# Performance work log

Measured on AMD Instinct MI355X. Metric: run time of the kernel, lower is better.

## Reference

```python
import jax, jax.numpy as jnp
import numpy as np

T, B = 64, 2048
LATENT, OBS, CTRL, NMAT, H = 128, 128, 16, 16, 128


def setup_inputs() -> dict:
    key = jax.random.key(0)
    ks = iter(jax.random.split(key, 32))

    def dense(shape, fan_in):
        return jax.random.normal(next(ks), shape, jnp.float32) / np.sqrt(fan_in)

    inp = {
        "xs": jax.random.normal(next(ks), (T, B, OBS), jnp.float32),
        "us": jax.random.normal(next(ks), (T, B, CTRL), jnp.float32),
        "eps1": jax.random.normal(next(ks), (B, LATENT), jnp.float32),
        "eps": jax.random.normal(next(ks), (T - 1, B, LATENT), jnp.float32),
        # InitialNetwork: LSTM(128) + Dense(128) + Dense(2*latent)
        "lstm_Wx": dense((OBS, 4 * H), OBS),
        "lstm_Wh": dense((H, 4 * H), H),
        "lstm_b": jnp.zeros((4 * H,), jnp.float32),
        "init_W1": dense((H, H), H),
        "init_b1": jnp.zeros((H,), jnp.float32),
        "init_W2": dense((H, 2 * LATENT), H),
        "init_b2": jnp.zeros((2 * LATENT,), jnp.float32),
        # InitialTransition
        "trans_W1": dense((LATENT, H), LATENT),
        "trans_b1": jnp.zeros((H,), jnp.float32),
        "trans_W2": dense((H, LATENT), H),
        "trans_b2": jnp.zeros((LATENT,), jnp.float32),
        # Observation
        "obs_W1": dense((LATENT, H), LATENT),
        "obs_b1": jnp.zeros((H,), jnp.float32),
        "obs_W2": dense((H, OBS), H),
        "obs_b2": jnp.zeros((OBS,), jnp.float32),
        # Recognition (input: z ++ x ++ u)
        "rec_W1": dense((LATENT + OBS + CTRL, H), LATENT + OBS + CTRL),
        "rec_b1": jnp.zeros((H,), jnp.float32),
        "rec_W2": dense((H, 2 * LATENT), H),
        "rec_b2": jnp.zeros((2 * LATENT,), jnp.float32),
        # TransitionWeights (no bias, normal(0.01) init)
        "alpha_W": 0.01 * jax.random.normal(next(ks), (LATENT + CTRL, NMAT), jnp.float32),
        # mixture banks
        "A": 0.01 * jax.random.normal(next(ks), (NMAT, LATENT, LATENT), jnp.float32),
        "Bm": 0.01 * jax.random.normal(next(ks), (NMAT, LATENT, CTRL), jnp.float32),
        "C": 0.01 * jax.random.normal(next(ks), (NMAT, OBS, LATENT), jnp.float32),
    }
    return inp


def reference(xs, us, eps1, eps, lstm_Wx, lstm_Wh, lstm_b,
              init_W1, init_b1, init_W2, init_b2,
              trans_W1, trans_b1, trans_W2, trans_b2,
              obs_W1, obs_b1, obs_W2, obs_b2,
              rec_W1, rec_b1, rec_W2, rec_b2,
              alpha_W, A, Bm, C):
    Bsz = xs.shape[1]
    Hd = lstm_Wh.shape[0]

    # --- InitialNetwork: LSTM over time (xs is (T,B,obs); flax transposes to batch-major, net effect is a scan over T) ---
    def lstm_step(carry, x_t):
        c, h = carry
        gates = x_t @ lstm_Wx + h @ lstm_Wh + lstm_b  # (B, 4H)
        i, f, g, o = jnp.split(gates, 4, axis=-1)     # flax gate order i,f,g,o
        c = jax.nn.sigmoid(f) * c + jax.nn.sigmoid(i) * jnp.tanh(g)
        h = jax.nn.sigmoid(o) * jnp.tanh(c)
        return (c, h), None

    zeros = jnp.zeros((Bsz, Hd), xs.dtype)
    (_, h_last), _ = jax.lax.scan(lstm_step, (zeros, zeros), xs)
    hid = jax.nn.relu(h_last @ init_W1 + init_b1)
    w1_mean, w1_logvar = jnp.split(hid @ init_W2 + init_b2, 2, axis=-1)
    w_1 = w1_mean + jnp.exp(w1_logvar / 2) * eps1

    # --- InitialTransition ---
    z_1 = jax.nn.relu(w_1 @ trans_W1 + trans_b1) @ trans_W2 + trans_b2

    def obs_fn(z):
        return jax.nn.relu(z @ obs_W1 + obs_b1) @ obs_W2 + obs_b2

    # --- unrolled DVBF transition as a scan over t = 0..T-2 ---
    def step(z, inp):
        x_next, u_t, eps_t = inp
        x_mean = obs_fn(z)
        r = jax.nn.relu(jnp.concatenate([z, x_next, u_t], axis=-1) @ rec_W1 + rec_b1)
        w_mean, w_logvar = jnp.split(r @ rec_W2 + rec_b2, 2, axis=-1)
        w = w_mean + jnp.exp(w_logvar / 2) * eps_t
        alphas = jax.nn.softmax(jnp.concatenate([z, u_t], axis=-1) @ alpha_W)  # (B, NMAT)
        # fused gating + matrix mixing + matvec (same math as building A_t/B_t/C_t)
        z_next = (jnp.einsum('bi,ijk,bk->bj', alphas, A, z)
                  + jnp.einsum('bi,ijk,bk->bj', alphas, Bm, u_t)
                  + jnp.einsum('bi,ijk,bk->bj', alphas, C, w))
        return z_next, (z_next, x_mean)

    Tn = xs.shape[0]
    _, (zs_rest, x_rec) = jax.lax.scan(step, z_1, (xs[1:], us[:Tn - 1], eps[:Tn - 1]))

    zs = jnp.concatenate([z_1[None], zs_rest], axis=0).reshape(-1, z_1.shape[-1])  # vstack -> (T*B, latent)
    x_rec = x_rec.reshape(-1, x_rec.shape[-1])                                    # ((T-1)*B, obs)
    return zs, x_rec
```

## Files before the change

### kernel.cpp

```cpp
#include <hip/hip_runtime.h>
#include <math.h>

#define TT   64
#define BB   2048
#define OBSN 128
#define CTRLN 16
#define LATN 128
#define NMN  16
#define HDN  128

typedef __attribute__((ext_vector_type(8))) short short8;
typedef __attribute__((ext_vector_type(4))) float f32x4;

__device__ __forceinline__ float sigf(float x) { return 1.0f / (1.0f + expf(-x)); }

__device__ __forceinline__ unsigned short f2bf(float x) {
    unsigned int u = __float_as_uint(x);
    unsigned int r = (u + 0x7fffu + ((u >> 16) & 1u)) >> 16;
    return (unsigned short)r;
}

__device__ __forceinline__ f32x4 mfma16(short8 a, short8 b, f32x4 c) {
    return __builtin_amdgcn_mfma_f32_16x16x32_bf16(a, b, c, 0, 0, 0);
}

__global__ __launch_bounds__(256) void cvt_bf4_k(
    const float* __restrict__ in, unsigned short* __restrict__ out, int n4)
{
    int i = blockIdx.x * 256 + threadIdx.x;
    if (i >= n4) return;
    float4 v = ((const float4*)in)[i];
    ushort4 o;
    o.x = f2bf(v.x); o.y = f2bf(v.y); o.z = f2bf(v.z); o.w = f2bf(v.w);
    ((ushort4*)out)[i] = o;
}

__global__ __launch_bounds__(256) void pack_b_k(
    const float* __restrict__ W, unsigned short* __restrict__ out,
    int K, int N, int KT)
{
    int id = blockIdx.x * 256 + threadIdx.x;
    int total = (N / 16) * KT * 64;
    if (id >= total) return;
    int lane = id & 63;
    int kt = (id >> 6) % KT;
    int nt = id / (64 * KT);
    int n = nt * 16 + (lane & 15);
    int kb = kt * 32 + (lane >> 4) * 8;
#pragma unroll
    for (int j = 0; j < 8; j++) {
        int k = kb + j;
        out[(size_t)id * 8 + j] = (k < K) ? f2bf(W[(size_t)k * N + n]) : (unsigned short)0;
    }
}

__global__ __launch_bounds__(256) void pack_lstm_k(
    const float* __restrict__ Wx, const float* __restrict__ Wh,
    unsigned short* __restrict__ out)
{
    int id = blockIdx.x * 256 + threadIdx.x;
    if (id >= 32 * 8 * 64) return;
    int lane = id & 63;
    int kt = (id >> 6) & 7;
    int nt = id >> 9;
    int n = nt * 16 + (lane & 15);
    int kb = kt * 32 + (lane >> 4) * 8;
#pragma unroll
    for (int j = 0; j < 8; j++) {
        int k = kb + j;
        float v = (k < 128) ? Wx[(size_t)k * 512 + n] : Wh[(size_t)(k - 128) * 512 + n];
        out[(size_t)id * 8 + j] = f2bf(v);
    }
}

__global__ __launch_bounds__(256) void pack_wmix_k(
    const float* __restrict__ A, const float* __restrict__ Bm,
    const float* __restrict__ C, unsigned short* __restrict__ out)
{
    int id = blockIdx.x * 256 + threadIdx.x;
    if (id >= 128 * 9 * 64) return;
    int lane = id & 63;
    int kt = (id >> 6) % 9;
    int nt = id / (64 * 9);
    int c = nt * 16 + (lane & 15);
    int i = c >> 7, jj = c & 127;
    int kb = kt * 32 + (lane >> 4) * 8;
#pragma unroll
    for (int j = 0; j < 8; j++) {
        int k = kb + j;
        float v;
        if (k < 128)      v = A[((size_t)(i * 128 + jj)) * 128 + k];
        else if (k < 144) v = Bm[(size_t)(i * 128 + jj) * 16 + (k - 128)];
        else if (k < 272) v = C[(size_t)(i * 128 + jj) * 128 + (k - 144)];
        else              v = 0.f;
        out[(size_t)id * 8 + j] = f2bf(v);
    }
}

__global__ __launch_bounds__(512) void lstm_k(
    const unsigned short* __restrict__ xs_bf,
    const unsigned short* __restrict__ lstm_pk,
    const float* __restrict__ bias,
    float* __restrict__ hlast)
{
    __shared__ unsigned short h_bf[16][136];
    __shared__ float cs[16][128];
    __shared__ float gb[16][516];
    __shared__ float bs[512];

    const int tid = threadIdx.x;
    const int lane = tid & 63;
    const int w = tid >> 6;
    const int quad = lane >> 4;
    const int l15 = lane & 15;
    const int row0 = blockIdx.x * 16;

    bs[tid] = bias[tid];
    for (int idx = tid; idx < 16 * 136; idx += 512) h_bf[idx / 136][idx % 136] = 0;
    for (int idx = tid; idx < 2048; idx += 512) cs[idx >> 7][idx & 127] = 0.f;
    __syncthreads();

    for (int t = 0; t < TT; t++) {
        short8 a[8];
#pragma unroll
        for (int kt = 0; kt < 4; kt++)
            a[kt] = *(const short8*)&xs_bf[((size_t)t * 2048 + row0 + l15) * 128 + kt * 32 + quad * 8];
#pragma unroll
        for (int kt = 4; kt < 8; kt++)
            a[kt] = *(const short8*)&h_bf[l15][(kt - 4) * 32 + quad * 8];

        f32x4 D[4];
#pragma unroll
        for (int s = 0; s < 4; s++) D[s] = (f32x4){0.f, 0.f, 0.f, 0.f};
#pragma unroll
        for (int kt = 0; kt < 8; kt++) {
#pragma unroll
            for (int s = 0; s < 4; s++) {
                int ntg = w * 4 + s;
                short8 b = *(const short8*)&lstm_pk[(((size_t)ntg * 8 + kt) * 64 + lane) * 8];
                D[s] = mfma16(a[kt], b, D[s]);
            }
        }
#pragma unroll
        for (int s = 0; s < 4; s++)
#pragma unroll
            for (int rg = 0; rg < 4; rg++)
                gb[quad * 4 + rg][(w * 4 + s) * 16 + l15] = D[s][rg];
        __syncthreads();

#pragma unroll
        for (int e = 0; e < 4; e++) {
            int idx = tid + e * 512;
            int r = idx >> 7, j = idx & 127;
            float gi = gb[r][j] + bs[j];
            float gf = gb[r][128 + j] + bs[128 + j];
            float gg = gb[r][256 + j] + bs[256 + j];
            float go = gb[r][384 + j] + bs[384 + j];
            float c = sigf(gf) * cs[r][j] + sigf(gi) * tanhf(gg);
            float h = sigf(go) * tanhf(c);
            cs[r][j] = c;
            h_bf[r][j] = f2bf(h);
            if (t == TT - 1) hlast[(size_t)(row0 + r) * 128 + j] = h;
        }
        __syncthreads();
    }
}

__global__ __launch_bounds__(512) void scan_k(
    const unsigned short* __restrict__ xs_bf,
    const unsigned short* __restrict__ us_bf,
    const float* __restrict__ eps,
    const unsigned short* __restrict__ rec1_pk,
    const float* __restrict__ rec_b1,
    const unsigned short* __restrict__ rec2_pk,
    const float* __restrict__ rec_b2,
    const unsigned short* __restrict__ alpha_pk,
    const unsigned short* __restrict__ wmix_pk,
    float* __restrict__ zs)
{
    __shared__ unsigned short amix[16][296];
    __shared__ unsigned short rb_bf[16][136];
    __shared__ float wv[16][260];
    __shared__ float part[8][16][132];
    __shared__ float logits[16][20];
    __shared__ float alph[16][20];
    __shared__ float b1s[128];
    __shared__ float b2s[256];

    const int tid = threadIdx.x;
    const int lane = tid & 63;
    const int w = tid >> 6;
    const int quad = lane >> 4;
    const int l15 = lane & 15;
    const int row0 = blockIdx.x * 16;

    if (tid < 128) b1s[tid] = rec_b1[tid];
    if (tid < 256) b2s[tid] = rec_b2[tid];
    for (int idx = tid; idx < 256; idx += 512)
        amix[idx >> 4][272 + (idx & 15)] = 0;
    for (int idx = tid; idx < 2048; idx += 512) {
        int r = idx >> 7, j = idx & 127;
        amix[r][j] = f2bf(zs[(size_t)(row0 + r) * 128 + j]);
    }
    __syncthreads();

    for (int t = 0; t < TT - 1; t++) {
        if (tid < 256) {
            int r = tid >> 4, c = tid & 15;
            amix[r][128 + c] = us_bf[((size_t)t * 2048 + row0 + r) * 16 + c];
        }
        __syncthreads();

        {
            short8 a[9];
#pragma unroll
            for (int kt = 0; kt < 4; kt++)
                a[kt] = *(const short8*)&amix[l15][kt * 32 + quad * 8];
#pragma unroll
            for (int kt = 4; kt < 8; kt++)
                a[kt] = *(const short8*)&xs_bf[((size_t)(t + 1) * 2048 + row0 + l15) * 128 + (kt - 4) * 32 + quad * 8];
            {
                short8 zz = {0, 0, 0, 0, 0, 0, 0, 0};
                a[8] = (quad < 2) ? *(const short8*)&amix[l15][128 + quad * 8] : zz;
            }
            f32x4 D = {0.f, 0.f, 0.f, 0.f};
#pragma unroll
            for (int kt = 0; kt < 9; kt++) {
                short8 b = *(const short8*)&rec1_pk[(((size_t)w * 9 + kt) * 64 + lane) * 8];
                D = mfma16(a[kt], b, D);
            }
            int col = w * 16 + l15;
#pragma unroll
            for (int rg = 0; rg < 4; rg++) {
                float v = fmaxf(D[rg] + b1s[col], 0.f);
                rb_bf[quad * 4 + rg][col] = f2bf(v);
            }
        }
        __syncthreads();

        {
            short8 a[4];
#pragma unroll
            for (int kt = 0; kt < 4; kt++)
                a[kt] = *(const short8*)&rb_bf[l15][kt * 32 + quad * 8];
            f32x4 D0 = {0.f, 0.f, 0.f, 0.f}, D1 = {0.f, 0.f, 0.f, 0.f};
            const int nt0 = w * 2, nt1 = w * 2 + 1;
#pragma unroll
            for (int kt = 0; kt < 4; kt++) {
                short8 b0 = *(const short8*)&rec2_pk[(((size_t)nt0 * 4 + kt) * 64 + lane) * 8];
                short8 b1 = *(const short8*)&rec2_pk[(((size_t)nt1 * 4 + kt) * 64 + lane) * 8];
                D0 = mfma16(a[kt], b0, D0);
                D1 = mfma16(a[kt], b1, D1);
            }
#pragma unroll
            for (int rg = 0; rg < 4; rg++) {
                wv[quad * 4 + rg][nt0 * 16 + l15] = D0[rg];
                wv[quad * 4 + rg][nt1 * 16 + l15] = D1[rg];
            }
            if (w == 7) {
                short8 az[5];
#pragma unroll
                for (int kt = 0; kt < 4; kt++)
                    az[kt] = *(const short8*)&amix[l15][kt * 32 + quad * 8];
                short8 zz = {0, 0, 0, 0, 0, 0, 0, 0};
                az[4] = (quad < 2) ? *(const short8*)&amix[l15][128 + quad * 8] : zz;
                f32x4 DL = {0.f, 0.f, 0.f, 0.f};
#pragma unroll
                for (int kt = 0; kt < 5; kt++) {
                    short8 b = *(const short8*)&alpha_pk[((size_t)kt * 64 + lane) * 8];
                    DL = mfma16(az[kt], b, DL);
                }
#pragma unroll
                for (int rg = 0; rg < 4; rg++)
                    logits[quad * 4 + rg][l15] = DL[rg];
            }
        }
        __syncthreads();

        if (tid < 16) {
            float m = -1e30f;
#pragma unroll
            for (int i = 0; i < 16; i++) m = fmaxf(m, logits[tid][i]);
            float ex[16];
            float s = 0.f;
#pragma unroll
            for (int i = 0; i < 16; i++) { ex[i] = expf(logits[tid][i] - m); s += ex[i]; }
            float inv = 1.f / s;
#pragma unroll
            for (int i = 0; i < 16; i++) alph[tid][i] = ex[i] * inv;
        }
#pragma unroll
        for (int e = 0; e < 4; e++) {
            int idx = tid + e * 512;
            int r = idx >> 7, j = idx & 127;
            float mv = wv[r][j] + b2s[j];
            float lv = wv[r][128 + j] + b2s[128 + j];
            float wval = mv + expf(0.5f * lv) * eps[((size_t)t * 2048 + row0 + r) * 128 + j];
            amix[r][144 + j] = f2bf(wval);
        }
        __syncthreads();

        {
            short8 a[9];
#pragma unroll
            for (int kt = 0; kt < 9; kt++)
                a[kt] = *(const short8*)&amix[l15][kt * 32 + quad * 8];
            const int i0 = 2 * w, i1 = 2 * w + 1;
            float a0[4], a1[4];
#pragma unroll
            for (int rg = 0; rg < 4; rg++) {
                a0[rg] = alph[quad * 4 + rg][i0];
                a1[rg] = alph[quad * 4 + rg][i1];
            }
#pragma unroll 1
            for (int jt = 0; jt < 8; jt++) {
                f32x4 D0 = {0.f, 0.f, 0.f, 0.f}, D1 = {0.f, 0.f, 0.f, 0.f};
#pragma unroll
                for (int kt = 0; kt < 9; kt++) {
                    short8 b0 = *(const short8*)&wmix_pk[((((size_t)i0 * 8 + jt) * 9 + kt) * 64 + lane) * 8];
                    short8 b1 = *(const short8*)&wmix_pk[((((size_t)i1 * 8 + jt) * 9 + kt) * 64 + lane) * 8];
                    D0 = mfma16(a[kt], b0, D0);
                    D1 = mfma16(a[kt], b1, D1);
                }
#pragma unroll
                for (int rg = 0; rg < 4; rg++)
                    part[w][quad * 4 + rg][jt * 16 + l15] = a0[rg] * D0[rg] + a1[rg] * D1[rg];
            }
        }
        __syncthreads();

#pragma unroll
        for (int e = 0; e < 4; e++) {
            int idx = tid + e * 512;
            int r = idx >> 7, j = idx & 127;
            float s = 0.f;
#pragma unroll
            for (int ww = 0; ww < 8; ww++) s += part[ww][r][j];
            zs[((size_t)(t + 1) * 2048 + row0 + r) * 128 + j] = s;
            amix[r][j] = f2bf(s);
        }
        __syncthreads();
    }
}

template <int RELU>
__global__ __launch_bounds__(256) void gemm_bias_k(
    const float* __restrict__ A, const float* __restrict__ W,
    const float* __restrict__ bias, float* __restrict__ Cout,
    int M, int K, int N)
{
    __shared__ float As[16][68];
    __shared__ float Ws[16][64];
    const int tid = threadIdx.x;
    const int row0 = blockIdx.x * 64;
    const int col0 = blockIdx.y * 64;
    const int tx = tid & 15, ty = tid >> 4;
    float acc[4][4];
#pragma unroll
    for (int a = 0; a < 4; a++)
#pragma unroll
        for (int b = 0; b < 4; b++) acc[a][b] = 0.f;

    for (int kc = 0; kc < K; kc += 16) {
        __syncthreads();
#pragma unroll
        for (int e = 0; e < 4; e++) {
            int idx = tid + e * 256;
            int r = idx >> 4, kk = idx & 15;
            As[kk][r] = A[(size_t)(row0 + r) * K + kc + kk];
        }
#pragma unroll
        for (int e = 0; e < 4; e++) {
            int idx = tid + e * 256;
            int kk = idx >> 6, jj = idx & 63;
            Ws[kk][jj] = W[(kc + kk) * N + col0 + jj];
        }
        __syncthreads();
#pragma unroll
        for (int kk = 0; kk < 16; kk++) {
            const float4 a4 = *(const float4*)&As[kk][ty * 4];
            const float4 w4 = *(const float4*)&Ws[kk][tx * 4];
            const float av[4] = {a4.x, a4.y, a4.z, a4.w};
            const float wv2[4] = {w4.x, w4.y, w4.z, w4.w};
#pragma unroll
            for (int r = 0; r < 4; r++)
#pragma unroll
                for (int j = 0; j < 4; j++) acc[r][j] += av[r] * wv2[j];
        }
    }
#pragma unroll
    for (int r = 0; r < 4; r++)
#pragma unroll
        for (int j = 0; j < 4; j++) {
            int gr = row0 + ty * 4 + r, gc = col0 + tx * 4 + j;
            float v = acc[r][j] + bias[gc];
            if (RELU) v = fmaxf(v, 0.f);
            Cout[(size_t)gr * N + gc] = v;
        }
}

__global__ __launch_bounds__(256) void gemm_meanvar_k(
    const float* __restrict__ A, const float* __restrict__ W,
    const float* __restrict__ bias, const float* __restrict__ eps,
    float* __restrict__ out)
{
    __shared__ float As[16][36];
    __shared__ float Ws[16][128];
    const int tid = threadIdx.x;
    const int row0 = blockIdx.x * 32;
    const int j0 = blockIdx.y * 64;
    const int tjx = tid & 31;
    const int trg = tid >> 5;
    float am[4][2], al[4][2];
#pragma unroll
    for (int a = 0; a < 4; a++) { am[a][0] = am[a][1] = 0.f; al[a][0] = al[a][1] = 0.f; }

    for (int kc = 0; kc < 128; kc += 16) {
        __syncthreads();
#pragma unroll
        for (int e = 0; e < 2; e++) {
            int idx = tid + e * 256;
            int r = idx >> 4, kk = idx & 15;
            As[kk][r] = A[(row0 + r) * 128 + kc + kk];
        }
#pragma unroll
        for (int e = 0; e < 2; e++) {
            int idx = tid + e * 256;
            int lin = idx * 4;
            int kk = lin >> 7, cc = lin & 127;
            int half = cc >> 6, jj = cc & 63;
            *(float4*)&Ws[kk][half * 64 + jj] =
                *(const float4*)(W + (kc + kk) * 256 + half * 128 + j0 + jj);
        }
        __syncthreads();
#pragma unroll
        for (int kk = 0; kk < 16; kk++) {
            const float4 a4 = *(const float4*)&As[kk][trg * 4];
            const float2 wm = *(const float2*)&Ws[kk][2 * tjx];
            const float2 wl = *(const float2*)&Ws[kk][64 + 2 * tjx];
            const float av[4] = {a4.x, a4.y, a4.z, a4.w};
#pragma unroll
            for (int rr = 0; rr < 4; rr++) {
                am[rr][0] += av[rr] * wm.x; am[rr][1] += av[rr] * wm.y;
                al[rr][0] += av[rr] * wl.x; al[rr][1] += av[rr] * wl.y;
            }
        }
    }
#pragma unroll
    for (int rr = 0; rr < 4; rr++)
#pragma unroll
        for (int jj = 0; jj < 2; jj++) {
            int r = row0 + trg * 4 + rr;
            int j = j0 + 2 * tjx + jj;
            float m = am[rr][jj] + bias[j];
            float l = al[rr][jj] + bias[128 + j];
            out[r * 128 + j] = m + expf(0.5f * l) * eps[r * 128 + j];
        }
}

__global__ __launch_bounds__(256) void mlp2_k(
    const float* __restrict__ Z, const float* __restrict__ W1,
    const float* __restrict__ b1, const float* __restrict__ W2,
    const float* __restrict__ b2, float* __restrict__ out)
{
    __shared__ float Zs[32][132];
    __shared__ float Hs[32][132];
    __shared__ float Ws[16][128];
    const int tid = threadIdx.x;
    const int row0 = blockIdx.x * 32;
    const int tx = tid & 31;
    const int ty = tid >> 5;

#pragma unroll
    for (int e = 0; e < 4; e++) {
        int idx = tid + e * 256;
        int lin = idx * 4;
        int r = lin >> 7, k = lin & 127;
        *(float4*)&Zs[r][k] = *(const float4*)(Z + (size_t)(row0 + r) * 128 + k);
    }

    float acc[4][4];
#pragma unroll
    for (int a = 0; a < 4; a++)
#pragma unroll
        for (int b = 0; b < 4; b++) acc[a][b] = 0.f;

    for (int kc = 0; kc < 128; kc += 16) {
        __syncthreads();
#pragma unroll
        for (int e = 0; e < 2; e++) {
            int idx = tid + e * 256;
            int lin = idx * 4;
            int kk = lin >> 7, j = lin & 127;
            *(float4*)&Ws[kk][j] = *(const float4*)(W1 + (kc + kk) * 128 + j);
        }
        __syncthreads();
#pragma unroll
        for (int kk = 0; kk < 16; kk++) {
            float av[4];
#pragma unroll
            for (int rr = 0; rr < 4; rr++) av[rr] = Zs[ty * 4 + rr][kc + kk];
            const float4 w4 = *(const float4*)&Ws[kk][tx * 4];
            const float wv2[4] = {w4.x, w4.y, w4.z, w4.w};
#pragma unroll
            for (int r = 0; r < 4; r++)
#pragma unroll
                for (int j = 0; j < 4; j++) acc[r][j] += av[r] * wv2[j];
        }
    }
#pragma unroll
    for (int rr = 0; rr < 4; rr++) {
        float4 hv;
        hv.x = fmaxf(acc[rr][0] + b1[tx * 4 + 0], 0.f);
        hv.y = fmaxf(acc[rr][1] + b1[tx * 4 + 1], 0.f);
        hv.z = fmaxf(acc[rr][2] + b1[tx * 4 + 2], 0.f);
        hv.w = fmaxf(acc[rr][3] + b1[tx * 4 + 3], 0.f);
        *(float4*)&Hs[ty * 4 + rr][tx * 4] = hv;
    }
#pragma unroll
    for (int a = 0; a < 4; a++)
#pragma unroll
        for (int b = 0; b < 4; b++) acc[a][b] = 0.f;

    for (int kc = 0; kc < 128; kc += 16) {
        __syncthreads();
#pragma unroll
        for (int e = 0; e < 2; e++) {
            int idx = tid + e * 256;
            int lin = idx * 4;
            int kk = lin >> 7, j = lin & 127;
            *(float4*)&Ws[kk][j] = *(const float4*)(W2 + (kc + kk) * 128 + j);
        }
        __syncthreads();
#pragma unroll
        for (int kk = 0; kk < 16; kk++) {
            float av[4];
#pragma unroll
            for (int rr = 0; rr < 4; rr++) av[rr] = Hs[ty * 4 + rr][kc + kk];
            const float4 w4 = *(const float4*)&Ws[kk][tx * 4];
            const float wv2[4] = {w4.x, w4.y, w4.z, w4.w};
#pragma unroll
            for (int r = 0; r < 4; r++)
#pragma unroll
                for (int j = 0; j < 4; j++) acc[r][j] += av[r] * wv2[j];
        }
    }
#pragma unroll
    for (int rr = 0; rr < 4; rr++) {
        float4 ov;
        ov.x = acc[rr][0] + b2[tx * 4 + 0];
        ov.y = acc[rr][1] + b2[tx * 4 + 1];
        ov.z = acc[rr][2] + b2[tx * 4 + 2];
        ov.w = acc[rr][3] + b2[tx * 4 + 3];
        *(float4*)(out + (size_t)(row0 + ty * 4 + rr) * 128 + tx * 4) = ov;
    }
}

extern "C" void kernel_launch(void* const* d_in, const int* in_sizes, int n_in,
                              void* d_out, int out_size, void* d_ws, size_t ws_size,
                              hipStream_t stream)
{
    (void)in_sizes; (void)n_in; (void)out_size; (void)ws_size;
    const float* xs       = (const float*)d_in[0];
    const float* us       = (const float*)d_in[1];
    const float* eps1     = (const float*)d_in[2];
    const float* eps      = (const float*)d_in[3];
    const float* lstm_Wx  = (const float*)d_in[4];
    const float* lstm_Wh  = (const float*)d_in[5];
    const float* lstm_b   = (const float*)d_in[6];
    const float* init_W1  = (const float*)d_in[7];
    const float* init_b1  = (const float*)d_in[8];
    const float* init_W2  = (const float*)d_in[9];
    const float* init_b2  = (const float*)d_in[10];
    const float* trans_W1 = (const float*)d_in[11];
    const float* trans_b1 = (const float*)d_in[12];
    const float* trans_W2 = (const float*)d_in[13];
    const float* trans_b2 = (const float*)d_in[14];
    const float* obs_W1   = (const float*)d_in[15];
    const float* obs_b1   = (const float*)d_in[16];
    const float* obs_W2   = (const float*)d_in[17];
    const float* obs_b2   = (const float*)d_in[18];
    const float* rec_W1   = (const float*)d_in[19];
    const float* rec_b1   = (const float*)d_in[20];
    const float* rec_W2   = (const float*)d_in[21];
    const float* rec_b2   = (const float*)d_in[22];
    const float* alpha_W  = (const float*)d_in[23];
    const float* Amat     = (const float*)d_in[24];
    const float* Bmat     = (const float*)d_in[25];
    const float* Cmat     = (const float*)d_in[26];

    float* out  = (float*)d_out;
    float* zs   = out;
    float* xrec = out + (size_t)TT * BB * LATN;

    char* ws = (char*)d_ws;
    unsigned short* xs_bf   = (unsigned short*)(ws);
    unsigned short* us_bf   = (unsigned short*)(ws + 33554432);
    unsigned short* lstm_pk = (unsigned short*)(ws + 37748736);
    unsigned short* rec1_pk = (unsigned short*)(ws + 38010880);
    unsigned short* rec2_pk = (unsigned short*)(ws + 38084608);
    unsigned short* alpha_pk= (unsigned short*)(ws + 38150144);
    unsigned short* wmix_pk = (unsigned short*)(ws + 38155264);
    float* hlast            = (float*)(ws + 39334912);
    float* hidb             = (float*)(ws + 40383488);
    float* w1b              = (float*)(ws + 41432064);
    float* rbg              = (float*)(ws + 42480640);

    cvt_bf4_k<<<16384, 256, 0, stream>>>(xs, xs_bf, 4194304);
    cvt_bf4_k<<<2048, 256, 0, stream>>>(us, us_bf, 524288);
    pack_lstm_k<<<64, 256, 0, stream>>>(lstm_Wx, lstm_Wh, lstm_pk);
    pack_b_k<<<18, 256, 0, stream>>>(rec_W1, rec1_pk, 272, 128, 9);
    pack_b_k<<<16, 256, 0, stream>>>(rec_W2, rec2_pk, 128, 256, 4);
    pack_b_k<<<2, 256, 0, stream>>>(alpha_W, alpha_pk, 144, 16, 5);
    pack_wmix_k<<<288, 256, 0, stream>>>(Amat, Bmat, Cmat, wmix_pk);

    lstm_k<<<128, 512, 0, stream>>>(xs_bf, lstm_pk, lstm_b, hlast);

    gemm_bias_k<1><<<dim3(32, 2), 256, 0, stream>>>(hlast, init_W1, init_b1, hidb, BB, 128, 128);
    gemm_meanvar_k<<<dim3(64, 2), 256, 0, stream>>>(hidb, init_W2, init_b2, eps1, w1b);
    gemm_bias_k<1><<<dim3(32, 2), 256, 0, stream>>>(w1b, trans_W1, trans_b1, rbg, BB, 128, 128);
    gemm_bias_k<0><<<dim3(32, 2), 256, 0, stream>>>(rbg, trans_W2, trans_b2, zs, BB, 128, 128);

    scan_k<<<128, 512, 0, stream>>>(xs_bf, us_bf, eps,
                                    rec1_pk, rec_b1, rec2_pk, rec_b2,
                                    alpha_pk, wmix_pk, zs);

    mlp2_k<<<dim3((TT - 1) * BB / 32), 256, 0, stream>>>(
        zs, obs_W1, obs_b1, obs_W2, obs_b2, xrec);
}
```

Measured before the change: 1.411 ms.

## Keep recurrent weights resident in registers/LDS and re-split mixture matmul by output tile

In the LSTM and scan kernels, the per-step weight fragments are loaded once into registers, with the overflow placed in LDS. This replaces global reloads on every timestep. The mixture matvec is repartitioned so each wave owns one 16-column output tile across all 16 matrices and accumulates the alpha-weighted sum locally. That removes the cross-wave partial-sum buffer, its reduction pass and one barrier per step. The xs and eps inputs are prefetched ahead of use, and the softmax is spread over 256 threads with shuffles. In exchange there is higher register and LDS pressure, and the mixture loop still streams most of its weights from global memory.

```diff
diff --git a/kernel.cpp b/kernel.cpp
--- a/kernel.cpp
+++ b/kernel.cpp
@@ -103,6 +103,7 @@
     const float* __restrict__ bias,
     float* __restrict__ hlast)
 {
+    __shared__ unsigned short wl[13 * 8 * 64 * 8];
     __shared__ unsigned short h_bf[16][136];
     __shared__ float cs[16][128];
     __shared__ float gb[16][516];
@@ -115,16 +116,33 @@
     const int l15 = lane & 15;
     const int row0 = blockIdx.x * 16;
 
+    short8 bl[19];
+#pragma unroll
+    for (int f = 0; f < 19; f++) {
+        int s = f >> 3, kt = f & 7;
+        bl[f] = *(const short8*)&lstm_pk[((((size_t)(w * 4 + s)) * 8 + kt) * 64 + lane) * 8];
+    }
+#pragma unroll
+    for (int f = 19; f < 32; f++) {
+        int s = f >> 3, kt = f & 7;
+        *(short8*)&wl[(((size_t)w * 13 + (f - 19)) * 64 + lane) * 8] =
+            *(const short8*)&lstm_pk[((((size_t)(w * 4 + s)) * 8 + kt) * 64 + lane) * 8];
+    }
+
     bs[tid] = bias[tid];
     for (int idx = tid; idx < 16 * 136; idx += 512) h_bf[idx / 136][idx % 136] = 0;
     for (int idx = tid; idx < 2048; idx += 512) cs[idx >> 7][idx & 127] = 0.f;
+
+    short8 axs[4];
+#pragma unroll
+    for (int kt = 0; kt < 4; kt++)
+        axs[kt] = *(const short8*)&xs_bf[((size_t)(row0 + l15)) * 128 + kt * 32 + quad * 8];
     __syncthreads();
 
     for (int t = 0; t < TT; t++) {
         short8 a[8];
 #pragma unroll
-        for (int kt = 0; kt < 4; kt++)
-            a[kt] = *(const short8*)&xs_bf[((size_t)t * 2048 + row0 + l15) * 128 + kt * 32 + quad * 8];
+        for (int kt = 0; kt < 4; kt++) a[kt] = axs[kt];
 #pragma unroll
         for (int kt = 4; kt < 8; kt++)
             a[kt] = *(const short8*)&h_bf[l15][(kt - 4) * 32 + quad * 8];
@@ -133,11 +151,13 @@
 #pragma unroll
         for (int s = 0; s < 4; s++) D[s] = (f32x4){0.f, 0.f, 0.f, 0.f};
 #pragma unroll
-        for (int kt = 0; kt < 8; kt++) {
-#pragma unroll
-            for (int s = 0; s < 4; s++) {
-                int ntg = w * 4 + s;
-                short8 b = *(const short8*)&lstm_pk[(((size_t)ntg * 8 + kt) * 64 + lane) * 8];
+        for (int s = 0; s < 4; s++) {
+#pragma unroll
+            for (int kt = 0; kt < 8; kt++) {
+                int f = s * 8 + kt;
+                short8 b;
+                if (f < 19) b = bl[f];
+                else        b = *(const short8*)&wl[(((size_t)w * 13 + (f - 19)) * 64 + lane) * 8];
                 D[s] = mfma16(a[kt], b, D[s]);
             }
         }
@@ -148,6 +168,11 @@
                 gb[quad * 4 + rg][(w * 4 + s) * 16 + l15] = D[s][rg];
         __syncthreads();
 
+        if (t + 1 < TT) {
+#pragma unroll
+            for (int kt = 0; kt < 4; kt++)
+                axs[kt] = *(const short8*)&xs_bf[((size_t)(t + 1) * 2048 + row0 + l15) * 128 + kt * 32 + quad * 8];
+        }
 #pragma unroll
         for (int e = 0; e < 4; e++) {
             int idx = tid + e * 512;
@@ -178,10 +203,10 @@
     const unsigned short* __restrict__ wmix_pk,
     float* __restrict__ zs)
 {
+    __shared__ unsigned short wlds[8 * 15 * 64 * 8];
     __shared__ unsigned short amix[16][296];
     __shared__ unsigned short rb_bf[16][136];
     __shared__ float wv[16][260];
-    __shared__ float part[8][16][132];
     __shared__ float logits[16][20];
     __shared__ float alph[16][20];
     __shared__ float b1s[128];
@@ -193,6 +218,24 @@
     const int quad = lane >> 4;
     const int l15 = lane & 15;
     const int row0 = blockIdx.x * 16;
+
+    short8 r1f[9];
+#pragma unroll
+    for (int kt = 0; kt < 9; kt++)
+        r1f[kt] = *(const short8*)&rec1_pk[(((size_t)w * 9 + kt) * 64 + lane) * 8];
+    short8 r2f[8];
+#pragma unroll
+    for (int s = 0; s < 2; s++)
+#pragma unroll
+        for (int kt = 0; kt < 4; kt++)
+            r2f[s * 4 + kt] = *(const short8*)&rec2_pk[((((size_t)(2 * w + s)) * 4 + kt) * 64 + lane) * 8];
+
+#pragma unroll
+    for (int f = 0; f < 15; f++) {
+        int i = f / 9, kt = f % 9;
+        *(short8*)&wlds[(((size_t)w * 15 + f) * 64 + lane) * 8] =
+            *(const short8*)&wmix_pk[((((size_t)i * 8 + w) * 9 + kt) * 64 + lane) * 8];
+    }
 
     if (tid < 128) b1s[tid] = rec_b1[tid];
     if (tid < 256) b2s[tid] = rec_b2[tid];
@@ -204,11 +247,23 @@
     }
     __syncthreads();
 
+    float ge[4];
+    short8 axs[4];
+
     for (int t = 0; t < TT - 1; t++) {
         if (tid < 256) {
             int r = tid >> 4, c = tid & 15;
             amix[r][128 + c] = us_bf[((size_t)t * 2048 + row0 + r) * 16 + c];
         }
+#pragma unroll
+        for (int e = 0; e < 4; e++) {
+            int idx = tid + e * 512;
+            int r = idx >> 7, j = idx & 127;
+            ge[e] = eps[((size_t)t * 2048 + row0 + r) * 128 + j];
+        }
+#pragma unroll
+        for (int kt = 0; kt < 4; kt++)
+            axs[kt] = *(const short8*)&xs_bf[((size_t)(t + 1) * 2048 + row0 + l15) * 128 + kt * 32 + quad * 8];
         __syncthreads();
 
         {
@@ -217,18 +272,15 @@
             for (int kt = 0; kt < 4; kt++)
                 a[kt] = *(const short8*)&amix[l15][kt * 32 + quad * 8];
 #pragma unroll
-            for (int kt = 4; kt < 8; kt++)
-                a[kt] = *(const short8*)&xs_bf[((size_t)(t + 1) * 2048 + row0 + l15) * 128 + (kt - 4) * 32 + quad * 8];
+            for (int kt = 4; kt < 8; kt++) a[kt] = axs[kt - 4];
             {
                 short8 zz = {0, 0, 0, 0, 0, 0, 0, 0};
                 a[8] = (quad < 2) ? *(const short8*)&amix[l15][128 + quad * 8] : zz;
             }
             f32x4 D = {0.f, 0.f, 0.f, 0.f};
 #pragma unroll
-            for (int kt = 0; kt < 9; kt++) {
-                short8 b = *(const short8*)&rec1_pk[(((size_t)w * 9 + kt) * 64 + lane) * 8];
-                D = mfma16(a[kt], b, D);
-            }
+            for (int kt = 0; kt < 9; kt++)
+                D = mfma16(a[kt], r1f[kt], D);
             int col = w * 16 + l15;
 #pragma unroll
             for (int rg = 0; rg < 4; rg++) {
@@ -244,18 +296,15 @@
             for (int kt = 0; kt < 4; kt++)
                 a[kt] = *(const short8*)&rb_bf[l15][kt * 32 + quad * 8];
             f32x4 D0 = {0.f, 0.f, 0.f, 0.f}, D1 = {0.f, 0.f, 0.f, 0.f};
-            const int nt0 = w * 2, nt1 = w * 2 + 1;
 #pragma unroll
             for (int kt = 0; kt < 4; kt++) {
-                short8 b0 = *(const short8*)&rec2_pk[(((size_t)nt0 * 4 + kt) * 64 + lane) * 8];
-                short8 b1 = *(const short8*)&rec2_pk[(((size_t)nt1 * 4 + kt) * 64 + lane) * 8];
-                D0 = mfma16(a[kt], b0, D0);
-                D1 = mfma16(a[kt], b1, D1);
+                D0 = mfma16(a[kt], r2f[kt], D0);
+                D1 = mfma16(a[kt], r2f[4 + kt], D1);
             }
 #pragma unroll
             for (int rg = 0; rg < 4; rg++) {
-                wv[quad * 4 + rg][nt0 * 16 + l15] = D0[rg];
-                wv[quad * 4 + rg][nt1 * 16 + l15] = D1[rg];
+                wv[quad * 4 + rg][(2 * w) * 16 + l15] = D0[rg];
+                wv[quad * 4 + rg][(2 * w + 1) * 16 + l15] = D1[rg];
             }
             if (w == 7) {
                 short8 az[5];
@@ -277,17 +326,19 @@
         }
         __syncthreads();
 
-        if (tid < 16) {
-            float m = -1e30f;
-#pragma unroll
-            for (int i = 0; i < 16; i++) m = fmaxf(m, logits[tid][i]);
-            float ex[16];
-            float s = 0.f;
-#pragma unroll
-            for (int i = 0; i < 16; i++) { ex[i] = expf(logits[tid][i] - m); s += ex[i]; }
-            float inv = 1.f / s;
-#pragma unroll
-            for (int i = 0; i < 16; i++) alph[tid][i] = ex[i] * inv;
+        if (tid < 256) {
+            int r = tid >> 4, i = tid & 15;
+            float x = logits[r][i];
+            float m = x;
+#pragma unroll
+            for (int off = 8; off > 0; off >>= 1)
+                m = fmaxf(m, __shfl_xor(m, off, 16));
+            float e = expf(x - m);
+            float s = e;
+#pragma unroll
+            for (int off = 8; off > 0; off >>= 1)
+                s += __shfl_xor(s, off, 16);
+            alph[r][i] = e / s;
         }
 #pragma unroll
         for (int e = 0; e < 4; e++) {
@@ -295,7 +346,7 @@
             int r = idx >> 7, j = idx & 127;
             float mv = wv[r][j] + b2s[j];
             float lv = wv[r][128 + j] + b2s[128 + j];
-            float wval = mv + expf(0.5f * lv) * eps[((size_t)t * 2048 + row0 + r) * 128 + j];
+            float wval = mv + expf(0.5f * lv) * ge[e];
             amix[r][144 + j] = f2bf(wval);
         }
         __syncthreads();
@@ -305,39 +356,31 @@
 #pragma unroll
             for (int kt = 0; kt < 9; kt++)
                 a[kt] = *(const short8*)&amix[l15][kt * 32 + quad * 8];
-            const int i0 = 2 * w, i1 = 2 * w + 1;
-            float a0[4], a1[4];
+            f32x4 acc = {0.f, 0.f, 0.f, 0.f};
+#pragma unroll
+            for (int i = 0; i < 16; i++) {
+                f32x4 D = {0.f, 0.f, 0.f, 0.f};
+#pragma unroll
+                for (int kt = 0; kt < 9; kt++) {
+                    int f = i * 9 + kt;
+                    short8 b;
+                    if (f < 15)
+                        b = *(const short8*)&wlds[(((size_t)w * 15 + f) * 64 + lane) * 8];
+                    else
+                        b = *(const short8*)&wmix_pk[((((size_t)i * 8 + w) * 9 + kt) * 64 + lane) * 8];
+                    D = mfma16(a[kt], b, D);
+                }
+#pragma unroll
+                for (int rg = 0; rg < 4; rg++)
+                    acc[rg] += alph[quad * 4 + rg][i] * D[rg];
+            }
 #pragma unroll
             for (int rg = 0; rg < 4; rg++) {
-                a0[rg] = alph[quad * 4 + rg][i0];
-                a1[rg] = alph[quad * 4 + rg][i1];
-            }
-#pragma unroll 1
-            for (int jt = 0; jt < 8; jt++) {
-                f32x4 D0 = {0.f, 0.f, 0.f, 0.f}, D1 = {0.f, 0.f, 0.f, 0.f};
-#pragma unroll
-                for (int kt = 0; kt < 9; kt++) {
-                    short8 b0 = *(const short8*)&wmix_pk[((((size_t)i0 * 8 + jt) * 9 + kt) * 64 + lane) * 8];
-                    short8 b1 = *(const short8*)&wmix_pk[((((size_t)i1 * 8 + jt) * 9 + kt) * 64 + lane) * 8];
-                    D0 = mfma16(a[kt], b0, D0);
-                    D1 = mfma16(a[kt], b1, D1);
-                }
-#pragma unroll
-                for (int rg = 0; rg < 4; rg++)
-                    part[w][quad * 4 + rg][jt * 16 + l15] = a0[rg] * D0[rg] + a1[rg] * D1[rg];
-            }
-        }
-        __syncthreads();
-
-#pragma unroll
-        for (int e = 0; e < 4; e++) {
-            int idx = tid + e * 512;
-            int r = idx >> 7, j = idx & 127;
-            float s = 0.f;
-#pragma unroll
-            for (int ww = 0; ww < 8; ww++) s += part[ww][r][j];
-            zs[((size_t)(t + 1) * 2048 + row0 + r) * 128 + j] = s;
-            amix[r][j] = f2bf(s);
+                int r = quad * 4 + rg;
+                float v = acc[rg];
+                zs[((size_t)(t + 1) * 2048 + row0 + r) * 128 + w * 16 + l15] = v;
+                amix[r][w * 16 + l15] = f2bf(v);
+            }
         }
         __syncthreads();
     }
```

Result: slower. 3.148 ms (+123.1%).
